# Kernel optimization log

Measured on AMD Instinct MI355X. Metric: run time of the kernel, lower is better.

Reference implementation:

```python
import jax, jax.numpy as jnp
import numpy as np

K, STRIDE, PAD, DIL = 3, 1, 1, 1
EPS = 1e-20


def kernel_channels(x):
    # x: [B, C, H, W] -> [B, C, K*K, H', W'] (row-major kernel ordering, as torch F.unfold)
    xp = jnp.pad(x, ((0, 0), (0, 0), (PAD, PAD), (PAD, PAD)))
    Hp, Wp = xp.shape[2], xp.shape[3]
    Ho = (Hp - DIL * (K - 1) - 1) // STRIDE + 1
    Wo = (Wp - DIL * (K - 1) - 1) // STRIDE + 1
    patches = [xp[:, :, i * DIL:i * DIL + (Ho - 1) * STRIDE + 1:STRIDE,
                       j * DIL:j * DIL + (Wo - 1) * STRIDE + 1:STRIDE]
               for i in range(K) for j in range(K)]
    return jnp.stack(patches, axis=2)


def setup_inputs() -> dict:
    key = jax.random.key(0)
    ks = jax.random.split(key, 8)
    B, Cin, Cout, H, W = 4, 32, 32, 256, 256
    d = jax.random.normal(ks[0], (B, Cin, H, W), jnp.float32)
    cd = jax.random.uniform(ks[1], (B, Cin, H, W), jnp.float32)          # confidences in [0,1)
    s = jax.random.uniform(ks[2], (B, Cin, H, W), jnp.float32)           # unused in forward (API compat)
    cs = jax.random.uniform(ks[3], (B, Cin, H, W), jnp.float32)          # unused in forward (API compat)
    s_prod_roll = jax.random.uniform(ks[4], (B, Cin, K * K, H, W), jnp.float32)
    channel_weight = jax.random.normal(ks[5], (Cout, Cin, 1, 1), jnp.float32)
    spatial_weight = jax.random.normal(ks[6], (Cin, 1, K * K, 1, 1), jnp.float32)
    bias = jax.random.normal(ks[7], (1, Cout, 1, 1), jnp.float32) * 0.01
    return {"d": d, "cd": cd, "s": s, "cs": cs, "s_prod_roll": s_prod_roll,
            "channel_weight": channel_weight, "spatial_weight": spatial_weight, "bias": bias}


def reference(d, cd, s, cs, s_prod_roll, channel_weight, spatial_weight, bias):
    # EnforcePos: weights are passed through softplus before use
    sw = jax.nn.softplus(spatial_weight)[:, 0, :, 0, 0]   # [Cin, K*K]
    cw = jax.nn.softplus(channel_weight)[:, :, 0, 0]      # [Cout, Cin]

    d_roll = kernel_channels(d)                            # [B, Cin, K*K, H, W]
    cd_roll = kernel_channels(cd)
    cd_prop = cd_roll * s_prod_roll

    # conv3d with groups=Cin, depth kernel K*K == per-channel weighted sum over neighbor axis
    nom = jnp.einsum('bckhw,ck->bchw', cd_prop * d_roll, sw)
    denom = jnp.einsum('bckhw,ck->bchw', cd_prop, sw)
    d_spatial = nom / (denom + EPS)
    cd_spatial = denom / jnp.sum(sw)

    # 1x1 conv2d, groups=1 == channel mixing
    nom2 = jnp.einsum('bchw,oc->bohw', cd_spatial * d_spatial, cw)
    denom2 = jnp.einsum('bchw,oc->bohw', cd_spatial, cw)
    d_out = nom2 / (denom2 + EPS) + bias
    cd_out = denom2 / jnp.sum(cw) / (STRIDE * STRIDE)
    return d_out, cd_out
```

## Files before the change

kernel.cpp:

```cpp
#include <hip/hip_runtime.h>

#define EPS 1e-20f
typedef float f4 __attribute__((ext_vector_type(4)));

__global__ void prep_weights(const float* __restrict__ channel_weight,
                             const float* __restrict__ spatial_weight,
                             float* __restrict__ ws) {
    __shared__ float red[256];
    int tid = threadIdx.x;
    float local_sw = 0.f, local_cw = 0.f;
    for (int i = tid; i < 288; i += 256) {
        float x = spatial_weight[i];
        float v = fmaxf(x, 0.f) + log1pf(expf(-fabsf(x)));
        ws[i] = v;
        local_sw += v;
    }
    for (int i = tid; i < 1024; i += 256) {
        float x = channel_weight[i];
        float v = fmaxf(x, 0.f) + log1pf(expf(-fabsf(x)));
        int o = i >> 5, c = i & 31;
        ws[288 + c * 32 + o] = v;
        local_cw += v;
    }
    red[tid] = local_sw;
    __syncthreads();
    for (int s = 128; s > 0; s >>= 1) {
        if (tid < s) red[tid] += red[tid + s];
        __syncthreads();
    }
    if (tid == 0) ws[1312] = 1.0f / red[0];
    __syncthreads();
    red[tid] = local_cw;
    __syncthreads();
    for (int s = 128; s > 0; s >>= 1) {
        if (tid < s) red[tid] += red[tid + s];
        __syncthreads();
    }
    if (tid == 0) ws[1313] = 1.0f / red[0];
}

__global__ __launch_bounds__(256) void fused11(
    const float* __restrict__ d,
    const float* __restrict__ cd,
    const float* __restrict__ sp,
    const float* __restrict__ wsbuf,
    const float* __restrict__ bias,
    float* __restrict__ out)
{
    __shared__ float lt[32 * 128];
    __shared__ float lc[32 * 128];
    __shared__ float lcw[1024];

    const int plane = 65536;

    int bid = blockIdx.x;
    bid = (bid & 7) * 256 + (bid >> 3);

    const int ct = bid & 1;
    const int h  = (bid >> 1) & 255;
    const int b  = bid >> 9;

    const int tid = threadIdx.x;

    #pragma unroll
    for (int i = 0; i < 4; ++i) lcw[i * 256 + tid] = wsbuf[288 + i * 256 + tid];

    const int w    = tid >> 6;
    const int half = (tid >> 5) & 1;
    const int pq   = tid & 31;
    const int col0 = ct * 128 + pq * 4;
    const float inv_sum_sw = wsbuf[1312];
    const bool rowv0 = (h >= 1), rowv2 = (h <= 254);

    f4 A[9], B[9];

#define ISSUE_SP(BUF, ITER) do { \
    const int ci_ = w * 8 + (ITER) * 2 + half; \
    const float* __restrict__ spC_ = sp + (size_t)(b * 32 + ci_) * 9 * plane + h * 256; \
    _Pragma("unroll") \
    for (int k_ = 0; k_ < 9; ++k_) \
        BUF[k_] = __builtin_nontemporal_load((const f4*)(spC_ + (size_t)k_ * plane + col0)); \
} while (0)

#define COMPUTE_ITER(BUF, ITER, PREFETCH) do { \
    const int c_  = w * 8 + (ITER) * 2 + half; \
    const int bc_ = b * 32 + c_; \
    const float* __restrict__ dC_  = d  + (size_t)bc_ * plane; \
    const float* __restrict__ cdC_ = cd + (size_t)bc_ * plane; \
    float dr_[3][6], cr_[3][6]; \
    _Pragma("unroll") \
    for (int i_ = 0; i_ < 3; ++i_) { \
        const int hc_ = min(max(h + i_ - 1, 0), 255); \
        const float* __restrict__ drow_ = dC_ + hc_ * 256; \
        const float* __restrict__ crow_ = cdC_ + hc_ * 256; \
        f4 dv_ = *(const f4*)(drow_ + col0); \
        f4 cv_ = *(const f4*)(crow_ + col0); \
        dr_[i_][1] = dv_[0]; dr_[i_][2] = dv_[1]; dr_[i_][3] = dv_[2]; dr_[i_][4] = dv_[3]; \
        cr_[i_][1] = cv_[0]; cr_[i_][2] = cv_[1]; cr_[i_][3] = cv_[2]; cr_[i_][4] = cv_[3]; \
        dr_[i_][0] = drow_[max(col0 - 1, 0)]; \
        cr_[i_][0] = crow_[max(col0 - 1, 0)]; \
        dr_[i_][5] = drow_[min(col0 + 4, 255)]; \
        cr_[i_][5] = crow_[min(col0 + 4, 255)]; \
    } \
    PREFETCH; \
    float swk_[9]; \
    _Pragma("unroll") \
    for (int k_ = 0; k_ < 9; ++k_) swk_[k_] = wsbuf[c_ * 9 + k_]; \
    float nom_[4] = {0.f, 0.f, 0.f, 0.f}, den_[4] = {0.f, 0.f, 0.f, 0.f}; \
    _Pragma("unroll") \
    for (int i_ = 0; i_ < 3; ++i_) { \
        const bool rv_ = (i_ == 0) ? rowv0 : ((i_ == 2) ? rowv2 : true); \
        _Pragma("unroll") \
        for (int j_ = 0; j_ < 3; ++j_) { \
            const int k_ = i_ * 3 + j_; \
            const float s_ = swk_[k_]; \
            _Pragma("unroll") \
            for (int p_ = 0; p_ < 4; ++p_) { \
                const int ww_ = col0 + p_ + j_ - 1; \
                const bool valid_ = rv_ && ((unsigned)ww_ < 256u); \
                const float cdp_ = valid_ ? cr_[i_][p_ + j_] * BUF[k_][p_] : 0.f; \
                nom_[p_] = fmaf(cdp_ * dr_[i_][p_ + j_], s_, nom_[p_]); \
                den_[p_] = fmaf(cdp_, s_, den_[p_]); \
            } \
        } \
    } \
     \
    f4 tv_, cv4_; \
    _Pragma("unroll") \
    for (int p_ = 0; p_ < 4; ++p_) { \
        tv_[p_]  = nom_[p_] * inv_sum_sw; \
        cv4_[p_] = den_[p_] * inv_sum_sw; \
    } \
    *(f4*)&lt[c_ * 128 + pq * 4] = tv_; \
    *(f4*)&lc[c_ * 128 + pq * 4] = cv4_; \
} while (0)

    ISSUE_SP(A, 0);
    COMPUTE_ITER(A, 0, ISSUE_SP(B, 1));
    COMPUTE_ITER(B, 1, ISSUE_SP(A, 2));
    COMPUTE_ITER(A, 2, ISSUE_SP(B, 3));
    COMPUTE_ITER(B, 3, ((void)0));

#undef ISSUE_SP
#undef COMPUTE_ITER

    __syncthreads();

    const int og = tid >> 5;
    const int o0 = og * 4;

    float n2[4][4], d2[4][4];
    #pragma unroll
    for (int oi = 0; oi < 4; ++oi)
        #pragma unroll
        for (int j = 0; j < 4; ++j) { n2[oi][j] = 0.f; d2[oi][j] = 0.f; }

    for (int cc = 0; cc < 32; ++cc) {
        const f4 tq = *(const f4*)&lt[cc * 128 + pq * 4];
        const f4 cq = *(const f4*)&lc[cc * 128 + pq * 4];
        const f4 cw4 = *(const f4*)&lcw[cc * 32 + o0];
        #pragma unroll
        for (int oi = 0; oi < 4; ++oi)
            #pragma unroll
            for (int j = 0; j < 4; ++j) {
                n2[oi][j] = fmaf(tq[j], cw4[oi], n2[oi][j]);
                d2[oi][j] = fmaf(cq[j], cw4[oi], d2[oi][j]);
            }
    }

    const float inv_sum_cw = wsbuf[1313];
    const f4 b4 = *(const f4*)&bias[o0];
    const int colb = ct * 128 + pq * 4;

    #pragma unroll
    for (int oi = 0; oi < 4; ++oi) {
        f4 dv, cv;
        #pragma unroll
        for (int j = 0; j < 4; ++j) {
            dv[j] = n2[oi][j] / (d2[oi][j] + EPS) + b4[oi];
            cv[j] = d2[oi][j] * inv_sum_cw;
        }
        const size_t po = (size_t)(b * 32 + o0 + oi) * plane + h * 256 + colb;
        *(f4*)(out + po)           = dv;
        *(f4*)(out + 8388608 + po) = cv;
    }
}

extern "C" void kernel_launch(void* const* d_in, const int* in_sizes, int n_in,
                              void* d_out, int out_size, void* d_ws, size_t ws_size,
                              hipStream_t stream) {
    const float* d    = (const float*)d_in[0];
    const float* cd   = (const float*)d_in[1];
    const float* sp   = (const float*)d_in[4];
    const float* cwt  = (const float*)d_in[5];
    const float* swt  = (const float*)d_in[6];
    const float* bias = (const float*)d_in[7];
    float* out = (float*)d_out;
    float* ws  = (float*)d_ws;

    prep_weights<<<1, 256, 0, stream>>>(cwt, swt, ws);
    fused11<<<2048, 256, 0, stream>>>(d, cd, sp, ws, bias, out);
}
```

Before: 94.30 us.

## Process full rows per block, shuffle halo, interleave channel-mix with stencil

Each block now covers a whole 256-wide row, so there are 1024 blocks instead of 2048, and one wave64 spans the row with 4 columns per lane. The left and right halo values come from wave shuffles instead of extra scalar global loads. The d/cd rows are software-prefetched together with s_prod_roll across 8 double-buffered iterations. The 1x1 channel-mixing accumulation is interleaved with the stencil after each 4-channel group, each thread holding 8 outputs x 4 columns. This removes redundant halo loads and overlaps the mixing with memory traffic, at the cost of heavier register and LDS use, which can lower occupancy, plus one block barrier per iteration.

```diff
diff --git a/kernel.cpp b/kernel.cpp
--- a/kernel.cpp
+++ b/kernel.cpp
@@ -39,7 +39,7 @@
     if (tid == 0) ws[1313] = 1.0f / red[0];
 }
 
-__global__ __launch_bounds__(256) void fused11(
+__global__ __launch_bounds__(256) void fused13(
     const float* __restrict__ d,
     const float* __restrict__ cd,
     const float* __restrict__ sp,
@@ -47,18 +47,17 @@
     const float* __restrict__ bias,
     float* __restrict__ out)
 {
-    __shared__ float lt[32 * 128];
-    __shared__ float lc[32 * 128];
+    __shared__ float lt[32 * 256];
+    __shared__ float lc[32 * 256];
     __shared__ float lcw[1024];
 
     const int plane = 65536;
 
     int bid = blockIdx.x;
-    bid = (bid & 7) * 256 + (bid >> 3);
-
-    const int ct = bid & 1;
-    const int h  = (bid >> 1) & 255;
-    const int b  = bid >> 9;
+    bid = (bid & 7) * 128 + (bid >> 3);
+
+    const int h = bid & 255;
+    const int b = bid >> 8;
 
     const int tid = threadIdx.x;
 
@@ -66,43 +65,50 @@
     for (int i = 0; i < 4; ++i) lcw[i * 256 + tid] = wsbuf[288 + i * 256 + tid];
 
     const int w    = tid >> 6;
-    const int half = (tid >> 5) & 1;
-    const int pq   = tid & 31;
-    const int col0 = ct * 128 + pq * 4;
+    const int lane = tid & 63;
+    const int col0 = lane * 4;
     const float inv_sum_sw = wsbuf[1312];
     const bool rowv0 = (h >= 1), rowv2 = (h <= 254);
 
-    f4 A[9], B[9];
-
-#define ISSUE_SP(BUF, ITER) do { \
-    const int ci_ = w * 8 + (ITER) * 2 + half; \
-    const float* __restrict__ spC_ = sp + (size_t)(b * 32 + ci_) * 9 * plane + h * 256; \
+    f4 spA[9], spB[9], dA[3], dB[3], cA[3], cB[3];
+    f4 n2[8], d2[8];
+    #pragma unroll
+    for (int oi = 0; oi < 8; ++oi)
+        #pragma unroll
+        for (int j = 0; j < 4; ++j) { n2[oi][j] = 0.f; d2[oi][j] = 0.f; }
+
+#define ISSUE(SPB, DB, CB, ITER) do { \
+    const int ci_  = (ITER) * 4 + w; \
+    const int bci_ = b * 32 + ci_; \
+    const float* __restrict__ spC_ = sp + (size_t)bci_ * 9 * plane + h * 256 + col0; \
     _Pragma("unroll") \
     for (int k_ = 0; k_ < 9; ++k_) \
-        BUF[k_] = __builtin_nontemporal_load((const f4*)(spC_ + (size_t)k_ * plane + col0)); \
-} while (0)
-
-#define COMPUTE_ITER(BUF, ITER, PREFETCH) do { \
-    const int c_  = w * 8 + (ITER) * 2 + half; \
-    const int bc_ = b * 32 + c_; \
-    const float* __restrict__ dC_  = d  + (size_t)bc_ * plane; \
-    const float* __restrict__ cdC_ = cd + (size_t)bc_ * plane; \
-    float dr_[3][6], cr_[3][6]; \
+        SPB[k_] = __builtin_nontemporal_load((const f4*)(spC_ + (size_t)k_ * plane)); \
+    const float* __restrict__ dC_  = d  + (size_t)bci_ * plane; \
+    const float* __restrict__ cdC_ = cd + (size_t)bci_ * plane; \
     _Pragma("unroll") \
     for (int i_ = 0; i_ < 3; ++i_) { \
         const int hc_ = min(max(h + i_ - 1, 0), 255); \
-        const float* __restrict__ drow_ = dC_ + hc_ * 256; \
-        const float* __restrict__ crow_ = cdC_ + hc_ * 256; \
-        f4 dv_ = *(const f4*)(drow_ + col0); \
-        f4 cv_ = *(const f4*)(crow_ + col0); \
-        dr_[i_][1] = dv_[0]; dr_[i_][2] = dv_[1]; dr_[i_][3] = dv_[2]; dr_[i_][4] = dv_[3]; \
-        cr_[i_][1] = cv_[0]; cr_[i_][2] = cv_[1]; cr_[i_][3] = cv_[2]; cr_[i_][4] = cv_[3]; \
-        dr_[i_][0] = drow_[max(col0 - 1, 0)]; \
-        cr_[i_][0] = crow_[max(col0 - 1, 0)]; \
-        dr_[i_][5] = drow_[min(col0 + 4, 255)]; \
-        cr_[i_][5] = crow_[min(col0 + 4, 255)]; \
-    } \
-    PREFETCH; \
+        DB[i_] = *(const f4*)(dC_  + hc_ * 256 + col0); \
+        CB[i_] = *(const f4*)(cdC_ + hc_ * 256 + col0); \
+    } \
+} while (0)
+
+#define COMPUTE(SPB, DB, CB, ITER) do { \
+    const int c_ = (ITER) * 4 + w; \
+    float dr_[3][6], cr_[3][6]; \
+    _Pragma("unroll") \
+    for (int i_ = 0; i_ < 3; ++i_) { \
+        dr_[i_][0] = __shfl_up(DB[i_][3], 1); \
+        cr_[i_][0] = __shfl_up(CB[i_][3], 1); \
+        dr_[i_][5] = __shfl_down(DB[i_][0], 1); \
+        cr_[i_][5] = __shfl_down(CB[i_][0], 1); \
+        _Pragma("unroll") \
+        for (int p_ = 0; p_ < 4; ++p_) { \
+            dr_[i_][p_ + 1] = DB[i_][p_]; \
+            cr_[i_][p_ + 1] = CB[i_][p_]; \
+        } \
+    } \
     float swk_[9]; \
     _Pragma("unroll") \
     for (int k_ = 0; k_ < 9; ++k_) swk_[k_] = wsbuf[c_ * 9 + k_]; \
@@ -118,7 +124,7 @@
             for (int p_ = 0; p_ < 4; ++p_) { \
                 const int ww_ = col0 + p_ + j_ - 1; \
                 const bool valid_ = rv_ && ((unsigned)ww_ < 256u); \
-                const float cdp_ = valid_ ? cr_[i_][p_ + j_] * BUF[k_][p_] : 0.f; \
+                const float cdp_ = valid_ ? cr_[i_][p_ + j_] * SPB[k_][p_] : 0.f; \
                 nom_[p_] = fmaf(cdp_ * dr_[i_][p_ + j_], s_, nom_[p_]); \
                 den_[p_] = fmaf(cdp_, s_, den_[p_]); \
             } \
@@ -131,56 +137,57 @@
         tv_[p_]  = nom_[p_] * inv_sum_sw; \
         cv4_[p_] = den_[p_] * inv_sum_sw; \
     } \
-    *(f4*)&lt[c_ * 128 + pq * 4] = tv_; \
-    *(f4*)&lc[c_ * 128 + pq * 4] = cv4_; \
+    *(f4*)&lt[c_ * 256 + col0] = tv_; \
+    *(f4*)&lc[c_ * 256 + col0] = cv4_; \
 } while (0)
 
-    ISSUE_SP(A, 0);
-    COMPUTE_ITER(A, 0, ISSUE_SP(B, 1));
-    COMPUTE_ITER(B, 1, ISSUE_SP(A, 2));
-    COMPUTE_ITER(A, 2, ISSUE_SP(B, 3));
-    COMPUTE_ITER(B, 3, ((void)0));
-
-#undef ISSUE_SP
-#undef COMPUTE_ITER
-
-    __syncthreads();
-
-    const int og = tid >> 5;
-    const int o0 = og * 4;
-
-    float n2[4][4], d2[4][4];
+#define ACC(ITER) do { \
+    _Pragma("unroll") \
+    for (int cc_ = (ITER) * 4; cc_ < (ITER) * 4 + 4; ++cc_) { \
+        const f4 tq_  = *(const f4*)&lt[cc_ * 256 + col0]; \
+        const f4 cq_  = *(const f4*)&lc[cc_ * 256 + col0]; \
+        const f4 cwA_ = *(const f4*)&lcw[cc_ * 32 + w * 8]; \
+        const f4 cwB_ = *(const f4*)&lcw[cc_ * 32 + w * 8 + 4]; \
+        _Pragma("unroll") \
+        for (int oi_ = 0; oi_ < 4; ++oi_) { \
+            _Pragma("unroll") \
+            for (int j_ = 0; j_ < 4; ++j_) { \
+                n2[oi_][j_]     = fmaf(tq_[j_], cwA_[oi_], n2[oi_][j_]); \
+                d2[oi_][j_]     = fmaf(cq_[j_], cwA_[oi_], d2[oi_][j_]); \
+                n2[4 + oi_][j_] = fmaf(tq_[j_], cwB_[oi_], n2[4 + oi_][j_]); \
+                d2[4 + oi_][j_] = fmaf(cq_[j_], cwB_[oi_], d2[4 + oi_][j_]); \
+            } \
+        } \
+    } \
+} while (0)
+
+    ISSUE(spA, dA, cA, 0);
+    ISSUE(spB, dB, cB, 1); COMPUTE(spA, dA, cA, 0); __syncthreads(); ACC(0);
+    ISSUE(spA, dA, cA, 2); COMPUTE(spB, dB, cB, 1); __syncthreads(); ACC(1);
+    ISSUE(spB, dB, cB, 3); COMPUTE(spA, dA, cA, 2); __syncthreads(); ACC(2);
+    ISSUE(spA, dA, cA, 4); COMPUTE(spB, dB, cB, 3); __syncthreads(); ACC(3);
+    ISSUE(spB, dB, cB, 5); COMPUTE(spA, dA, cA, 4); __syncthreads(); ACC(4);
+    ISSUE(spA, dA, cA, 6); COMPUTE(spB, dB, cB, 5); __syncthreads(); ACC(5);
+    ISSUE(spB, dB, cB, 7); COMPUTE(spA, dA, cA, 6); __syncthreads(); ACC(6);
+                           COMPUTE(spB, dB, cB, 7); __syncthreads(); ACC(7);
+
+#undef ISSUE
+#undef COMPUTE
+#undef ACC
+
+    const float inv_sum_cw = wsbuf[1313];
+    const int o0 = w * 8;
+
     #pragma unroll
-    for (int oi = 0; oi < 4; ++oi)
-        #pragma unroll
-        for (int j = 0; j < 4; ++j) { n2[oi][j] = 0.f; d2[oi][j] = 0.f; }
-
-    for (int cc = 0; cc < 32; ++cc) {
-        const f4 tq = *(const f4*)&lt[cc * 128 + pq * 4];
-        const f4 cq = *(const f4*)&lc[cc * 128 + pq * 4];
-        const f4 cw4 = *(const f4*)&lcw[cc * 32 + o0];
-        #pragma unroll
-        for (int oi = 0; oi < 4; ++oi)
-            #pragma unroll
-            for (int j = 0; j < 4; ++j) {
-                n2[oi][j] = fmaf(tq[j], cw4[oi], n2[oi][j]);
-                d2[oi][j] = fmaf(cq[j], cw4[oi], d2[oi][j]);
-            }
-    }
-
-    const float inv_sum_cw = wsbuf[1313];
-    const f4 b4 = *(const f4*)&bias[o0];
-    const int colb = ct * 128 + pq * 4;
-
-    #pragma unroll
-    for (int oi = 0; oi < 4; ++oi) {
+    for (int oi = 0; oi < 8; ++oi) {
+        const float bo = bias[o0 + oi];
         f4 dv, cv;
         #pragma unroll
         for (int j = 0; j < 4; ++j) {
-            dv[j] = n2[oi][j] / (d2[oi][j] + EPS) + b4[oi];
+            dv[j] = n2[oi][j] / (d2[oi][j] + EPS) + bo;
             cv[j] = d2[oi][j] * inv_sum_cw;
         }
-        const size_t po = (size_t)(b * 32 + o0 + oi) * plane + h * 256 + colb;
+        const size_t po = (size_t)(b * 32 + o0 + oi) * plane + h * 256 + col0;
         *(f4*)(out + po)           = dv;
         *(f4*)(out + 8388608 + po) = cv;
     }
@@ -199,5 +206,5 @@
     float* ws  = (float*)d_ws;
 
     prep_weights<<<1, 256, 0, stream>>>(cwt, swt, ws);
-    fused11<<<2048, 256, 0, stream>>>(d, cd, sp, ws, bias, out);
+    fused13<<<1024, 256, 0, stream>>>(d, cd, sp, ws, bias, out);
 }
```

New measurement: 110.9 us. +17.6%, slower.
